# Kernel optimization log

Hardware: AMD Instinct MI355X
Metric: run time of the kernel (lower is better)

## Reference

```python
import jax, jax.numpy as jnp
import numpy as np

N = 64
EPS = 1e-8


def setup_inputs() -> dict:
    key = jax.random.key(0)
    k1, k2, k3 = jax.random.split(key, 3)
    x = jax.random.normal(k1, (524288, N), dtype=jnp.float32)
    L = jax.random.uniform(k2, (2 * N, 2 * N), dtype=jnp.float32)
    R = jax.random.uniform(k3, (N, N), dtype=jnp.float32)
    return {"x": x, "L": L, "R": R}


def reference(x, L, R):
    n = N
    xr = x.reshape(n, -1)                      # (n, T)
    M = L @ L.T + EPS * jnp.eye(2 * n, dtype=L.dtype)
    M11 = M[:n, :n]
    M21 = M[:n, n:]   # note: original code names M[:n, n:] as M21
    M22 = M[n:, n:]
    A = 2.0 * (M11 + M22 + R - R.T)            # (n, n)
    A = jnp.linalg.inv(A) @ M21                # Koopman operator (n, n)
    return (A @ xr).reshape(-1, n)
```

## Files before the change

### kernel.cpp

```cpp
#include <hip/hip_runtime.h>

#define SN 524288

typedef float f32x4 __attribute__((ext_vector_type(4)));

__global__ __launch_bounds__(256) void k_buildC(const float* __restrict__ L,
                                                const float* __restrict__ R,
                                                float* __restrict__ Ct) {
  __shared__ float4 Ls[4096];
  const float4* L4 = (const float4*)L;
  #pragma unroll
  for (int it = 0; it < 16; ++it) {
    int idx = threadIdx.x + it * 256;
    int row = idx >> 5, t4 = idx & 31;
    Ls[(row << 5) + (t4 ^ (row & 7))] = L4[idx];
  }
  __syncthreads();
  int g = blockIdx.x * 256 + threadIdx.x;
  int c = g >> 6;
  int i = g & 63;
  if (c < 64) {
    float d1 = 0.f, d2 = 0.f;
    #pragma unroll
    for (int t4 = 0; t4 < 32; ++t4) {
      float4 a1 = Ls[(i << 5) + (t4 ^ (i & 7))];
      float4 b1 = Ls[(c << 5) + (t4 ^ (c & 7))];
      float4 a2 = Ls[((64 + i) << 5) + (t4 ^ (i & 7))];
      float4 b2 = Ls[((64 + c) << 5) + (t4 ^ (c & 7))];
      d1 += a1.x * b1.x + a1.y * b1.y + a1.z * b1.z + a1.w * b1.w;
      d2 += a2.x * b2.x + a2.y * b2.y + a2.z * b2.z + a2.w * b2.w;
    }
    float val = 2.0f * (d1 + d2 + R[i * 64 + c] - R[c * 64 + i]);
    if (i == c) val += 4e-8f;
    Ct[c * 64 + i] = val;
  } else {
    int jj = c - 64;
    float d = 0.f;
    #pragma unroll
    for (int t4 = 0; t4 < 32; ++t4) {
      float4 a = Ls[(i << 5) + (t4 ^ (i & 7))];
      float4 b = Ls[((64 + jj) << 5) + (t4 ^ (jj & 7))];
      d += a.x * b.x + a.y * b.y + a.z * b.z + a.w * b.w;
    }
    Ct[c * 64 + i] = d;
  }
}

__global__ __launch_bounds__(256) void k_solve(const float* __restrict__ Ct,
                                               float* __restrict__ AtW) {
  __shared__ float colbuf[2][64];
  __shared__ __align__(16) float rowbuf[2][128];
  const int r = threadIdx.x & 63;
  const int cgrp = threadIdx.x >> 6;
  float creg[32];
  #pragma unroll
  for (int cc = 0; cc < 32; ++cc)
    creg[cc] = Ct[(cgrp * 32 + cc) * 64 + r];
  #pragma unroll
  for (int p = 0; p < 64; ++p) {
    const int pb = p & 1, pc = p >> 5, pi = p & 31;
    if (cgrp == pc) colbuf[pb][r] = creg[pi];
    if (r == p) {
      #pragma unroll
      for (int cc = 0; cc < 32; ++cc) rowbuf[pb][cgrp * 32 + cc] = creg[cc];
    }
    __syncthreads();
    const float f = colbuf[pb][r];
    const float inv = 1.0f / colbuf[pb][p];
    if (r == p) {
      #pragma unroll
      for (int cc = 0; cc < 32; ++cc) creg[cc] *= inv;
    } else {
      const float gg = f * inv;
      #pragma unroll
      for (int c4 = 0; c4 < 8; ++c4) {
        const float4 pv = *(const float4*)&rowbuf[pb][cgrp * 32 + c4 * 4];
        creg[c4 * 4 + 0] -= gg * pv.x;
        creg[c4 * 4 + 1] -= gg * pv.y;
        creg[c4 * 4 + 2] -= gg * pv.z;
        creg[c4 * 4 + 3] -= gg * pv.w;
      }
    }
  }
  if (cgrp >= 2) {
    #pragma unroll
    for (int cc = 0; cc < 32; ++cc) {
      int k = (cgrp - 2) * 32 + cc;
      AtW[((r >> 4) * 64 + k) * 16 + (r & 15)] = creg[cc];
    }
  }
}

__global__ __launch_bounds__(256) void k_apply(const float* __restrict__ x,
                                               const float* __restrict__ AtW,
                                               float* __restrict__ out) {
  const int lane = threadIdx.x & 63;
  const int h = __builtin_amdgcn_readfirstlane(threadIdx.x >> 6);
  const int c4 = blockIdx.x * 64 + lane;
  const float* __restrict__ Ab = AtW + h * 64 * 16;

  float acc[16][4];
  #pragma unroll
  for (int il = 0; il < 16; ++il)
    #pragma unroll
    for (int j = 0; j < 4; ++j) acc[il][j] = 0.f;

  const f32x4* x4 = (const f32x4*)x;
  f32x4 xb[8];
  #pragma unroll
  for (int d = 0; d < 8; ++d) xb[d] = x4[d * (SN / 4) + c4];

  #pragma unroll 8
  for (int k = 0; k < 64; ++k) {
    const f32x4 xv = xb[k & 7];
    const int kp = (k + 8 < 64) ? (k + 8) : 63;
    xb[k & 7] = x4[kp * (SN / 4) + c4];
    const float* __restrict__ ak = Ab + k * 16;
    #pragma unroll
    for (int il = 0; il < 16; ++il) {
      const float av = ak[il];
      acc[il][0] = fmaf(av, xv[0], acc[il][0]);
      acc[il][1] = fmaf(av, xv[1], acc[il][1]);
      acc[il][2] = fmaf(av, xv[2], acc[il][2]);
      acc[il][3] = fmaf(av, xv[3], acc[il][3]);
    }
  }

  f32x4* out4 = (f32x4*)out;
  #pragma unroll
  for (int il = 0; il < 16; ++il) {
    f32x4 v = {acc[il][0], acc[il][1], acc[il][2], acc[il][3]};
    out4[(h * 16 + il) * (SN / 4) + c4] = v;
  }
}

extern "C" void kernel_launch(void* const* d_in, const int* in_sizes, int n_in,
                              void* d_out, int out_size, void* d_ws, size_t ws_size,
                              hipStream_t stream) {
  const float* x = (const float*)d_in[0];
  const float* L = (const float*)d_in[1];
  const float* R = (const float*)d_in[2];
  float* out = (float*)d_out;
  float* Ct  = (float*)d_ws;
  float* AtW = Ct + 128 * 64;
  k_buildC<<<32, 256, 0, stream>>>(L, R, Ct);
  k_solve<<<1, 256, 0, stream>>>(Ct, AtW);
  k_apply<<<2048, 256, 0, stream>>>(x, AtW, out);
}
```

Before: 104.6 us.

## Share x tiles across waves via double-buffered LDS in apply kernel

Previously each of the four waves in a block loaded all 64 rows of its x column slice from global memory, so every x element was read four times. Now each wave loads a quarter of each 16-row chunk, stages it in a double-buffered LDS tile, and all waves read from shared memory. This cuts redundant global/L2 traffic for x. In exchange it adds 32KB of LDS per block, which may lower occupancy, plus a barrier per chunk.

New measurement: 126.4 us. +20.8%, slower.

```diff
diff --git a/kernel.cpp b/kernel.cpp
--- a/kernel.cpp
+++ b/kernel.cpp
@@ -94,44 +94,50 @@
 __global__ __launch_bounds__(256) void k_apply(const float* __restrict__ x,
                                                const float* __restrict__ AtW,
                                                float* __restrict__ out) {
+  __shared__ f32x4 xt[2][1024];
   const int lane = threadIdx.x & 63;
-  const int h = __builtin_amdgcn_readfirstlane(threadIdx.x >> 6);
+  const int w = threadIdx.x >> 6;
+  const int h = __builtin_amdgcn_readfirstlane(w);
   const int c4 = blockIdx.x * 64 + lane;
   const float* __restrict__ Ab = AtW + h * 64 * 16;
+  const f32x4* x4 = (const f32x4*)x;
 
-  float acc[16][4];
+  f32x4 acc[16];
   #pragma unroll
-  for (int il = 0; il < 16; ++il)
+  for (int il = 0; il < 16; ++il) acc[il] = (f32x4){0.f, 0.f, 0.f, 0.f};
+
+  f32x4 st[4];
+  #pragma unroll
+  for (int s = 0; s < 4; ++s) st[s] = x4[(s * 4 + w) * (SN / 4) + c4];
+  #pragma unroll
+  for (int s = 0; s < 4; ++s) xt[0][(s * 4 + w) * 64 + lane] = st[s];
+
+  for (int c = 0; c < 4; ++c) {
+    __syncthreads();
+    if (c < 3) {
+      #pragma unroll
+      for (int s = 0; s < 4; ++s)
+        st[s] = x4[((c + 1) * 16 + s * 4 + w) * (SN / 4) + c4];
+    }
     #pragma unroll
-    for (int j = 0; j < 4; ++j) acc[il][j] = 0.f;
-
-  const f32x4* x4 = (const f32x4*)x;
-  f32x4 xb[8];
-  #pragma unroll
-  for (int d = 0; d < 8; ++d) xb[d] = x4[d * (SN / 4) + c4];
-
-  #pragma unroll 8
-  for (int k = 0; k < 64; ++k) {
-    const f32x4 xv = xb[k & 7];
-    const int kp = (k + 8 < 64) ? (k + 8) : 63;
-    xb[k & 7] = x4[kp * (SN / 4) + c4];
-    const float* __restrict__ ak = Ab + k * 16;
-    #pragma unroll
-    for (int il = 0; il < 16; ++il) {
-      const float av = ak[il];
-      acc[il][0] = fmaf(av, xv[0], acc[il][0]);
-      acc[il][1] = fmaf(av, xv[1], acc[il][1]);
-      acc[il][2] = fmaf(av, xv[2], acc[il][2]);
-      acc[il][3] = fmaf(av, xv[3], acc[il][3]);
+    for (int kk = 0; kk < 16; ++kk) {
+      const f32x4 xv = xt[c & 1][kk * 64 + lane];
+      const float* __restrict__ ak = Ab + (c * 16 + kk) * 16;
+      #pragma unroll
+      for (int il = 0; il < 16; ++il)
+        acc[il] += ak[il] * xv;
+    }
+    if (c < 3) {
+      #pragma unroll
+      for (int s = 0; s < 4; ++s)
+        xt[(c + 1) & 1][(s * 4 + w) * 64 + lane] = st[s];
     }
   }
 
   f32x4* out4 = (f32x4*)out;
   #pragma unroll
-  for (int il = 0; il < 16; ++il) {
-    f32x4 v = {acc[il][0], acc[il][1], acc[il][2], acc[il][3]};
-    out4[(h * 16 + il) * (SN / 4) + c4] = v;
-  }
+  for (int il = 0; il < 16; ++il)
+    out4[(h * 16 + il) * (SN / 4) + c4] = acc[il];
 }
 
 extern "C" void kernel_launch(void* const* d_in, const int* in_sizes, int n_in,
```
